# Performance work log

Hardware: AMD Instinct MI355X
Metric: run time of the kernel (lower is better)

Reference implementation:

```python
import jax, jax.numpy as jnp
import numpy as np

N = 4096        # batch size (rows)
K = 4           # instances per class -> num_instances in the torch code
D = 256         # embedding dim
MARGIN = 0.5
SAMPLE_KEY = jax.random.key(42)  # fixed key: deterministic stand-in for torch.multinomial


def setup_inputs() -> dict:
    key = jax.random.key(0)
    x = jax.random.normal(key, (N, D), dtype=jnp.float32)
    # L2-normalize like typical metric-learning embeddings so sims are in [-1, 1]
    inputs = x / jnp.linalg.norm(x, axis=1, keepdims=True)
    targets = (jnp.arange(N) // K).astype(jnp.int32)  # P*K batch: equal-size classes
    return {"inputs": inputs, "targets": targets}


def reference(inputs, targets):
    n = inputs.shape[0]
    km1 = K - 1                 # positives per row
    n_neg = n - K               # negatives per row

    sim = inputs @ inputs.T                                   # [n, n]
    same = targets[:, None] == targets[None, :]
    eye = jnp.eye(n, dtype=bool)
    pos_mask = same & ~eye
    neg_mask = ~same

    # masked_select + per-row sort: masked entries -> +inf, ascending sort,
    # keep first count entries (counts are uniform across rows)
    pos_sorted = jnp.sort(jnp.where(pos_mask, sim, jnp.inf), axis=1)[:, :km1]   # [n, K-1]
    neg_sorted = jnp.sort(jnp.where(neg_mask, sim, jnp.inf), axis=1)[:, :n_neg] # [n, n-K]

    pos_d = jnp.mean(pos_sorted)
    neg_d = jnp.mean(neg_sorted)

    # GaussDistribution per row over negatives
    neg_mean = jnp.mean(neg_sorted, axis=1, keepdims=True)
    neg_std = jnp.sqrt(jnp.mean((neg_sorted - neg_mean) ** 2, axis=1, keepdims=True))
    # NOTE: the original uses exp(+(x-mu)^2 / (2 sigma^2)) (no minus sign) -- faithful
    logprob = (neg_sorted - neg_mean) ** 2 / (2.0 * neg_std ** 2)               # [n, n-K]

    # multinomial without replacement ~ Gumbel top-k on log-weights
    gumbel = -jnp.log(-jnp.log(
        jax.random.uniform(SAMPLE_KEY, logprob.shape, minval=1e-20, maxval=1.0)))
    _, neg_idx = jax.lax.top_k(logprob + gumbel, km1)                            # [n, K-1]
    neg_pair = jnp.take_along_axis(neg_sorted, neg_idx, axis=1)                  # [n, K-1]

    pos_loss = jnp.mean(jnp.log1p(jnp.exp(-2.0 * (pos_sorted - MARGIN))), axis=1)
    neg_loss = 0.04 * jnp.mean(jnp.log1p(jnp.exp(50.0 * (neg_pair - MARGIN))), axis=1)
    loss = jnp.sum(pos_loss + neg_loss) / n

    # prec: fraction of rows where hardest positive > hardest sampled negative + 0.05
    c = jnp.sum(pos_sorted[:, -1] > jnp.max(neg_pair, axis=1) + 0.05)
    prec = c.astype(jnp.float32) / n

    return loss, prec, pos_d, neg_d
```

## Files before the change

kernel.cpp:

```cpp
#include <hip/hip_runtime.h>
#include <hip/hip_bf16.h>
#include <cstdint>
#include <cfloat>
#include <math.h>

#define NN 4096
#define DD 256
#define NNEG 4092
#define MARGIN 0.5f
#define NB 3584
#define NW (NB / 2)

__device__ __forceinline__ uint32_t rotl32(uint32_t x, int r) {
  return (x << r) | (x >> (32 - r));
}

__device__ __forceinline__ void threefry2x32_42(uint32_t x0, uint32_t x1,
                                                uint32_t& o0, uint32_t& o1) {
  const uint32_t k0 = 0u, k1 = 42u;
  const uint32_t k2 = k0 ^ k1 ^ 0x1BD11BDAu;
  x0 += k0; x1 += k1;
#define TF_R(r) { x0 += x1; x1 = rotl32(x1, r); x1 ^= x0; }
  TF_R(13) TF_R(15) TF_R(26) TF_R(6)
  x0 += k1; x1 += k2 + 1u;
  TF_R(17) TF_R(29) TF_R(16) TF_R(24)
  x0 += k2; x1 += k0 + 2u;
  TF_R(13) TF_R(15) TF_R(26) TF_R(6)
  x0 += k0; x1 += k1 + 3u;
  TF_R(17) TF_R(29) TF_R(16) TF_R(24)
  x0 += k1; x1 += k2 + 4u;
  TF_R(13) TF_R(15) TF_R(26) TF_R(6)
  x0 += k2; x1 += k0 + 5u;
#undef TF_R
  o0 = x0; o1 = x1;
}

__device__ __forceinline__ float gumbel_at(uint32_t f) {
  uint32_t o0, o1;
  threefry2x32_42(0u, f, o0, o1);
  uint32_t bits = o0 ^ o1;
  uint32_t fb = (bits >> 9) | 0x3F800000u;
  float fl = __uint_as_float(fb) - 1.0f;
  float u = fmaxf(1e-20f, fl + 1e-20f);
  return -logf(-logf(u));
}

__device__ __forceinline__ int bucket_of(float v) {
  return (int)fminf(fmaxf((v + 0.5f) * (float)NB, 0.0f), (float)(NB - 1));
}

#define BT 128
#define NT (NN / BT)
#define BK 32
#define LDSS 36
#define GEMM_BLOCKS (NT * (NT + 1) / 2)
#define GUMBEL_BLOCKS 240
#define GTOTAL ((uint32_t)NN * (uint32_t)NNEG)

__global__ __launch_bounds__(256) void gemm_gumbel(const float* __restrict__ X,
                                                   float* __restrict__ S,
                                                   float* __restrict__ G) {
  __shared__ float As[BT * LDSS];
  __shared__ float Bs[BT * LDSS];
  const int tid = threadIdx.x;

  if (blockIdx.x >= GEMM_BLOCKS) {
    uint32_t i = (uint32_t)(blockIdx.x - GEMM_BLOCKS) * 256u + (uint32_t)tid;
    const uint32_t stride = (uint32_t)GUMBEL_BLOCKS * 256u;
    for (; i < GTOTAL; i += stride) G[i] = gumbel_at(i);
    return;
  }

  const int tx = tid & 15, ty = tid >> 4;

  int b = blockIdx.x, bi = 0;
  while (b >= NT - bi) { b -= NT - bi; bi++; }
  const int bj = bi + b;
  const int rowBase = bi * BT, colBase = bj * BT;

  float acc[8][8] = {};
  for (int kb = 0; kb < DD; kb += BK) {
#pragma unroll
    for (int it = 0; it < 4; ++it) {
      int idx = tid + 256 * it;
      int r = idx >> 3, c4 = idx & 7;
      float4 av = *(const float4*)(X + (size_t)(rowBase + r) * DD + kb + c4 * 4);
      float4 bv = *(const float4*)(X + (size_t)(colBase + r) * DD + kb + c4 * 4);
      *(float4*)(As + r * LDSS + c4 * 4) = av;
      *(float4*)(Bs + r * LDSS + c4 * 4) = bv;
    }
    __syncthreads();
    for (int k = 0; k < BK; k += 4) {
      float4 a[8], bfr[8];
#pragma unroll
      for (int i = 0; i < 8; ++i) a[i] = *(const float4*)(As + (ty + 16 * i) * LDSS + k);
#pragma unroll
      for (int j = 0; j < 8; ++j) bfr[j] = *(const float4*)(Bs + (tx + 16 * j) * LDSS + k);
#pragma unroll
      for (int i = 0; i < 8; ++i)
#pragma unroll
        for (int j = 0; j < 8; ++j) {
          acc[i][j] += a[i].x * bfr[j].x;
          acc[i][j] += a[i].y * bfr[j].y;
          acc[i][j] += a[i].z * bfr[j].z;
          acc[i][j] += a[i].w * bfr[j].w;
        }
    }
    __syncthreads();
  }
#pragma unroll
  for (int i = 0; i < 8; ++i)
#pragma unroll
    for (int j = 0; j < 8; ++j)
      S[(size_t)(rowBase + ty + 16 * i) * NN + colBase + tx + 16 * j] = acc[i][j];
  if (bi != bj) {
#pragma unroll
    for (int i = 0; i < 8; ++i)
#pragma unroll
      for (int j = 0; j < 8; ++j)
        S[(size_t)(colBase + tx + 16 * j) * NN + rowBase + ty + 16 * i] = acc[i][j];
  }
}

#define INSERT3(sc, v)                                              \
  if ((sc) > s2) {                                                  \
    if ((sc) > s1) {                                                \
      s2 = s1; v2 = v1;                                             \
      if ((sc) > s0) { s1 = s0; v1 = v0; s0 = (sc); v0 = (v); }     \
      else           { s1 = (sc); v1 = (v); }                       \
    } else { s2 = (sc); v2 = (v); }                                 \
  }

template <int USE_G>
__global__ __launch_bounds__(256) void row_kernel(const float* __restrict__ S,
                                                  const float* __restrict__ G,
                                                  float* __restrict__ acc) {
  __shared__ uint32_t histw[NW];
  __shared__ uint32_t offsw[NW];
  __shared__ float sval[NN];
  __shared__ float sh[48];
  __shared__ uint32_t wtot[4];

  const int row = blockIdx.x;
  const int tid = threadIdx.x;
  const int lane = tid & 63, wid = tid >> 6;

#pragma unroll
  for (int i = 0; i < 7; ++i) histw[tid + 256 * i] = 0u;

  const float4* src = (const float4*)(S + (size_t)row * NN);
  const int pslot = row >> 2;
  float vv[16];
#pragma unroll
  for (int it = 0; it < 4; ++it) {
    int slot = tid + 256 * it;
    float4 t4 = src[slot];
    if (slot == pslot) {
      sh[16] = t4.x; sh[17] = t4.y; sh[18] = t4.z; sh[19] = t4.w;
      t4.x = INFINITY; t4.y = INFINITY; t4.z = INFINITY; t4.w = INFINITY;
    }
    vv[4 * it + 0] = t4.x; vv[4 * it + 1] = t4.y;
    vv[4 * it + 2] = t4.z; vv[4 * it + 3] = t4.w;
  }

  float s = 0.0f;
#pragma unroll
  for (int e = 0; e < 16; ++e) if (vv[e] < 1e30f) s += vv[e];
#pragma unroll
  for (int off = 32; off > 0; off >>= 1) s += __shfl_down(s, off, 64);
  if (lane == 0) sh[5 + wid] = s;
  __syncthreads();

#pragma unroll
  for (int e = 0; e < 16; ++e) {
    int b = bucket_of(vv[e]);
    atomicAdd(&histw[b >> 1], 1u << ((b & 1) << 4));
  }
  if (tid == 0) {
    int self = row & 3;
    float p[3]; int m = 0;
#pragma unroll
    for (int c = 0; c < 4; ++c)
      if (c != self) p[m++] = sh[16 + c];
    float t;
    if (p[0] > p[1]) { t = p[0]; p[0] = p[1]; p[1] = t; }
    if (p[1] > p[2]) { t = p[1]; p[1] = p[2]; p[2] = t; }
    if (p[0] > p[1]) { t = p[0]; p[0] = p[1]; p[1] = t; }
    sh[0] = p[0]; sh[1] = p[1]; sh[2] = p[2];
    float tot = sh[5] + sh[6] + sh[7] + sh[8];
    sh[9] = tot;
    sh[3] = tot / (float)NNEG;
  }
  __syncthreads();

  uint32_t hw[7];
  uint32_t s14 = 0;
#pragma unroll
  for (int j = 0; j < 7; ++j) {
    hw[j] = histw[7 * tid + j];
    s14 += (hw[j] & 0xFFFFu) + (hw[j] >> 16);
  }
  uint32_t inc = s14;
#pragma unroll
  for (int off = 1; off < 64; off <<= 1) {
    uint32_t n = __shfl_up(inc, (unsigned)off, 64);
    if (lane >= off) inc += n;
  }
  if (lane == 63) wtot[wid] = inc;

  const float mu = sh[3];
  float q = 0.0f;
#pragma unroll
  for (int e = 0; e < 16; ++e)
    if (vv[e] < 1e30f) { float d = vv[e] - mu; q += d * d; }
#pragma unroll
  for (int off = 32; off > 0; off >>= 1) q += __shfl_down(q, off, 64);
  if (lane == 0) sh[10 + wid] = q;
  __syncthreads();

  uint32_t wbase = 0;
  for (int w = 0; w < wid; ++w) wbase += wtot[w];
  uint32_t run = wbase + inc - s14;
#pragma unroll
  for (int j = 0; j < 7; ++j) {
    uint32_t lo = run; run += hw[j] & 0xFFFFu;
    uint32_t hi = run; run += hw[j] >> 16;
    offsw[7 * tid + j] = lo | (hi << 16);
  }
  if (tid == 0) {
    float var = (sh[10] + sh[11] + sh[12] + sh[13]) / (float)NNEG;
    float sd = sqrtf(var);
    sh[4] = 1.0f / (2.0f * sd * sd);
  }
  __syncthreads();

#pragma unroll
  for (int e = 0; e < 16; ++e) {
    int b = bucket_of(vv[e]);
    uint32_t old = atomicAdd(&offsw[b >> 1], 1u << ((b & 1) << 4));
    uint32_t sl = (old >> ((b & 1) << 4)) & 0xFFFFu;
    sval[sl] = vv[e];
  }
  __syncthreads();

  const float inv2s2 = sh[4];
  const uint32_t fbase = (uint32_t)row * (uint32_t)NNEG;
  const float* __restrict__ Grow = G + fbase;
  float s0 = -FLT_MAX, s1 = -FLT_MAX, s2 = -FLT_MAX;
  float v0 = 0.0f, v1 = 0.0f, v2 = 0.0f;
  float vr[16]; uint32_t cr[16];
#pragma unroll
  for (int it = 0; it < 16; ++it) {
    int sl = tid + 256 * it;
    float v = sval[sl];
    uint32_t cnt = 0u;
    if (v < 1e30f) {
      int b = bucket_of(v);
      uint32_t sh16 = (uint32_t)((b & 1) << 4);
      uint32_t end = (offsw[b >> 1] >> sh16) & 0xFFFFu;
      uint32_t cntb = (histw[b >> 1] >> sh16) & 0xFFFFu;
      uint32_t st = end - cntb;
      int c = (int)st;
      for (uint32_t u = st; u < end; ++u) {
        float w = sval[u];
        c += (w < v || (w == v && (int)u < sl)) ? 1 : 0;
      }
      cnt = (uint32_t)c;
    }
    vr[it] = v; cr[it] = cnt;
  }

#pragma unroll
  for (int it = 0; it < 16; ++it) {
    float v = vr[it];
    if (v < 1e30f) {
      float g = USE_G ? Grow[cr[it]] : gumbel_at(fbase + cr[it]);
      float d = v - mu;
      float sc = d * d * inv2s2 + g;
      INSERT3(sc, v)
    }
  }

#pragma unroll
  for (int dlt = 1; dlt < 64; dlt <<= 1) {
    float t0 = __shfl_xor(s0, dlt, 64), u0 = __shfl_xor(v0, dlt, 64);
    float t1 = __shfl_xor(s1, dlt, 64), u1 = __shfl_xor(v1, dlt, 64);
    float t2 = __shfl_xor(s2, dlt, 64), u2 = __shfl_xor(v2, dlt, 64);
    INSERT3(t0, u0)
    INSERT3(t1, u1)
    INSERT3(t2, u2)
  }
  if (lane == 0) {
    int b0 = 24 + wid * 6;
    sh[b0 + 0] = s0; sh[b0 + 1] = v0;
    sh[b0 + 2] = s1; sh[b0 + 3] = v1;
    sh[b0 + 4] = s2; sh[b0 + 5] = v2;
  }
  __syncthreads();

  if (tid == 0) {
    float g0 = -FLT_MAX, g1 = -FLT_MAX, g2 = -FLT_MAX;
    float w0 = 0.0f, w1 = 0.0f, w2 = 0.0f;
    {
      float s0 = g0, s1 = g1, s2 = g2, v0 = w0, v1 = w1, v2 = w2;
#pragma unroll
      for (int i = 0; i < 12; ++i) {
        float sc = sh[24 + 2 * i], v = sh[24 + 2 * i + 1];
        INSERT3(sc, v)
      }
      g0 = s0; g1 = s1; g2 = s2; w0 = v0; w1 = v1; w2 = v2;
    }
    float negmax = fmaxf(w0, fmaxf(w1, w2));
    float neg_loss = 0.04f * (log1pf(expf(50.0f * (w0 - MARGIN))) +
                              log1pf(expf(50.0f * (w1 - MARGIN))) +
                              log1pf(expf(50.0f * (w2 - MARGIN)))) / 3.0f;
    float p0 = sh[0], p1 = sh[1], p2 = sh[2];
    float pos_loss = (log1pf(expf(-2.0f * (p0 - MARGIN))) +
                      log1pf(expf(-2.0f * (p1 - MARGIN))) +
                      log1pf(expf(-2.0f * (p2 - MARGIN)))) / 3.0f;
    atomicAdd(&acc[0], pos_loss + neg_loss);
    if (p2 > negmax + 0.05f) atomicAdd(&acc[1], 1.0f);
    atomicAdd(&acc[2], p0 + p1 + p2);
    atomicAdd(&acc[3], sh[9]);
  }
}

__global__ void finalize(const float* __restrict__ acc, float* out) {
  if (threadIdx.x == 0 && blockIdx.x == 0) {
    out[0] = acc[0] / 4096.0f;
    out[1] = acc[1] / 4096.0f;
    out[2] = acc[2] / (4096.0f * 3.0f);
    out[3] = acc[3] / (4096.0f * 4092.0f);
  }
}

extern "C" void kernel_launch(void* const* d_in, const int* in_sizes, int n_in,
                              void* d_out, int out_size, void* d_ws, size_t ws_size,
                              hipStream_t stream) {
  (void)in_sizes; (void)n_in; (void)out_size;
  const float* X = (const float*)d_in[0];
  float* S = (float*)d_ws;
  float* acc = (float*)((char*)d_ws + (size_t)NN * NN * 4);
  float* G = (float*)((char*)d_ws + (size_t)NN * NN * 4 + 256);
  const size_t need = (size_t)NN * NN * 4 + 256 + (size_t)GTOTAL * 4;
  const bool have_g = ws_size >= need;

  hipMemsetAsync(acc, 0, 4 * sizeof(float), stream);
  if (have_g) {
    gemm_gumbel<<<GEMM_BLOCKS + GUMBEL_BLOCKS, 256, 0, stream>>>(X, S, G);
    row_kernel<1><<<NN, 256, 0, stream>>>(S, G, acc);
  } else {
    gemm_gumbel<<<GEMM_BLOCKS, 256, 0, stream>>>(X, S, G);
    row_kernel<0><<<NN, 256, 0, stream>>>(S, G, acc);
  }
  finalize<<<1, 64, 0, stream>>>(acc, (float*)d_out);
}
```

Measured before the change: 374.8 us.

## Shrink GEMM tiles, front-load Gumbel blocks, narrow buckets, vectorize rank scan

The symmetric GEMM tile drops from 128 to 64 with a deeper K slice, producing many more, smaller blocks. Gumbel-generation blocks move to the front of the grid and their count rises. The bucket mapping now covers a narrower value range [-0.28, 0.28] at higher resolution, which shrinks per-bucket scan lengths, and the within-bucket rank count reads float4s from LDS and is fused with the Gumbel lookup and top-3 insert. The narrow bucket range assumes the similarity distribution of the test inputs; values outside it are clamped into the edge buckets, which still stays correct but scans more there.

```diff
diff --git a/kernel.cpp b/kernel.cpp
--- a/kernel.cpp
+++ b/kernel.cpp
@@ -10,6 +10,7 @@
 #define MARGIN 0.5f
 #define NB 3584
 #define NW (NB / 2)
+#define GTOTAL ((uint32_t)NN * (uint32_t)NNEG)
 
 __device__ __forceinline__ uint32_t rotl32(uint32_t x, int r) {
   return (x << r) | (x >> (32 - r));
@@ -46,17 +47,17 @@
 }
 
 __device__ __forceinline__ int bucket_of(float v) {
-  return (int)fminf(fmaxf((v + 0.5f) * (float)NB, 0.0f), (float)(NB - 1));
-}
-
-#define BT 128
-#define NT (NN / BT)
-#define BK 32
-#define LDSS 36
-#define GEMM_BLOCKS (NT * (NT + 1) / 2)
-#define GUMBEL_BLOCKS 240
-#define GTOTAL ((uint32_t)NN * (uint32_t)NNEG)
-
+  return (int)fminf(fmaxf((v + 0.28f) * 6400.0f, 0.0f), (float)(NB - 1));
+}
+
+#define BT 64
+#define NTT (NN / BT)
+#define GEMM_BLOCKS (NTT * (NTT + 1) / 2)
+#define BK 64
+#define LDSS 68
+#define GUMBEL_BLOCKS 384
+
+template <int GOFF>
 __global__ __launch_bounds__(256) void gemm_gumbel(const float* __restrict__ X,
                                                    float* __restrict__ S,
                                                    float* __restrict__ G) {
@@ -64,26 +65,26 @@
   __shared__ float Bs[BT * LDSS];
   const int tid = threadIdx.x;
 
-  if (blockIdx.x >= GEMM_BLOCKS) {
-    uint32_t i = (uint32_t)(blockIdx.x - GEMM_BLOCKS) * 256u + (uint32_t)tid;
-    const uint32_t stride = (uint32_t)GUMBEL_BLOCKS * 256u;
+  if (GOFF > 0 && (int)blockIdx.x < GOFF) {
+    uint32_t i = (uint32_t)blockIdx.x * 256u + (uint32_t)tid;
+    const uint32_t stride = (uint32_t)GOFF * 256u;
     for (; i < GTOTAL; i += stride) G[i] = gumbel_at(i);
     return;
   }
 
   const int tx = tid & 15, ty = tid >> 4;
 
-  int b = blockIdx.x, bi = 0;
-  while (b >= NT - bi) { b -= NT - bi; bi++; }
+  int b = (int)blockIdx.x - GOFF, bi = 0;
+  while (b >= NTT - bi) { b -= NTT - bi; bi++; }
   const int bj = bi + b;
   const int rowBase = bi * BT, colBase = bj * BT;
 
-  float acc[8][8] = {};
+  float acc[4][4] = {};
   for (int kb = 0; kb < DD; kb += BK) {
 #pragma unroll
     for (int it = 0; it < 4; ++it) {
       int idx = tid + 256 * it;
-      int r = idx >> 3, c4 = idx & 7;
+      int r = idx >> 4, c4 = idx & 15;
       float4 av = *(const float4*)(X + (size_t)(rowBase + r) * DD + kb + c4 * 4);
       float4 bv = *(const float4*)(X + (size_t)(colBase + r) * DD + kb + c4 * 4);
       *(float4*)(As + r * LDSS + c4 * 4) = av;
@@ -91,15 +92,15 @@
     }
     __syncthreads();
     for (int k = 0; k < BK; k += 4) {
-      float4 a[8], bfr[8];
-#pragma unroll
-      for (int i = 0; i < 8; ++i) a[i] = *(const float4*)(As + (ty + 16 * i) * LDSS + k);
-#pragma unroll
-      for (int j = 0; j < 8; ++j) bfr[j] = *(const float4*)(Bs + (tx + 16 * j) * LDSS + k);
-#pragma unroll
-      for (int i = 0; i < 8; ++i)
-#pragma unroll
-        for (int j = 0; j < 8; ++j) {
+      float4 a[4], bfr[4];
+#pragma unroll
+      for (int i = 0; i < 4; ++i) a[i] = *(const float4*)(As + (ty + 16 * i) * LDSS + k);
+#pragma unroll
+      for (int j = 0; j < 4; ++j) bfr[j] = *(const float4*)(Bs + (tx + 16 * j) * LDSS + k);
+#pragma unroll
+      for (int i = 0; i < 4; ++i)
+#pragma unroll
+        for (int j = 0; j < 4; ++j) {
           acc[i][j] += a[i].x * bfr[j].x;
           acc[i][j] += a[i].y * bfr[j].y;
           acc[i][j] += a[i].z * bfr[j].z;
@@ -109,15 +110,15 @@
     __syncthreads();
   }
 #pragma unroll
-  for (int i = 0; i < 8; ++i)
-#pragma unroll
-    for (int j = 0; j < 8; ++j)
+  for (int i = 0; i < 4; ++i)
+#pragma unroll
+    for (int j = 0; j < 4; ++j)
       S[(size_t)(rowBase + ty + 16 * i) * NN + colBase + tx + 16 * j] = acc[i][j];
   if (bi != bj) {
 #pragma unroll
-    for (int i = 0; i < 8; ++i)
-#pragma unroll
-      for (int j = 0; j < 8; ++j)
+    for (int i = 0; i < 4; ++i)
+#pragma unroll
+      for (int j = 0; j < 4; ++j)
         S[(size_t)(colBase + tx + 16 * j) * NN + rowBase + ty + 16 * i] = acc[i][j];
   }
 }
@@ -137,7 +138,7 @@
                                                   float* __restrict__ acc) {
   __shared__ uint32_t histw[NW];
   __shared__ uint32_t offsw[NW];
-  __shared__ float sval[NN];
+  __shared__ __align__(16) float sval[NN];
   __shared__ float sh[48];
   __shared__ uint32_t wtot[4];
 
@@ -248,36 +249,61 @@
   const float* __restrict__ Grow = G + fbase;
   float s0 = -FLT_MAX, s1 = -FLT_MAX, s2 = -FLT_MAX;
   float v0 = 0.0f, v1 = 0.0f, v2 = 0.0f;
-  float vr[16]; uint32_t cr[16];
+
+  float va[16]; uint32_t sten[16];
+#pragma unroll
+  for (int it = 0; it < 16; ++it) va[it] = sval[tid + 256 * it];
 #pragma unroll
   for (int it = 0; it < 16; ++it) {
-    int sl = tid + 256 * it;
-    float v = sval[sl];
-    uint32_t cnt = 0u;
+    float v = va[it];
+    uint32_t pk = 0u;
     if (v < 1e30f) {
       int b = bucket_of(v);
       uint32_t sh16 = (uint32_t)((b & 1) << 4);
       uint32_t end = (offsw[b >> 1] >> sh16) & 0xFFFFu;
-      uint32_t cntb = (histw[b >> 1] >> sh16) & 0xFFFFu;
-      uint32_t st = end - cntb;
-      int c = (int)st;
-      for (uint32_t u = st; u < end; ++u) {
-        float w = sval[u];
-        c += (w < v || (w == v && (int)u < sl)) ? 1 : 0;
+      uint32_t cb = (histw[b >> 1] >> sh16) & 0xFFFFu;
+      pk = (end - cb) | (end << 16);
+    }
+    sten[it] = pk;
+  }
+
+#pragma unroll
+  for (int half = 0; half < 2; ++half) {
+    float4 w0[8];
+#pragma unroll
+    for (int j = 0; j < 8; ++j) {
+      uint32_t st = sten[half * 8 + j] & 0xFFFFu;
+      w0[j] = *(const float4*)(sval + (st & ~3u));
+    }
+#pragma unroll
+    for (int j = 0; j < 8; ++j) {
+      const int it = half * 8 + j;
+      float v = va[it];
+      if (v < 1e30f) {
+        const int sl = tid + 256 * it;
+        const uint32_t st = sten[it] & 0xFFFFu, en = sten[it] >> 16;
+        const uint32_t nb = en - st;
+        const uint32_t u0 = st & ~3u;
+        int cnt = (int)st;
+        {
+          float4 w = w0[j];
+          cnt += ((u0 + 0 - st) < nb && (w.x < v || (w.x == v && (int)(u0 + 0) < sl))) ? 1 : 0;
+          cnt += ((u0 + 1 - st) < nb && (w.y < v || (w.y == v && (int)(u0 + 1) < sl))) ? 1 : 0;
+          cnt += ((u0 + 2 - st) < nb && (w.z < v || (w.z == v && (int)(u0 + 2) < sl))) ? 1 : 0;
+          cnt += ((u0 + 3 - st) < nb && (w.w < v || (w.w == v && (int)(u0 + 3) < sl))) ? 1 : 0;
+        }
+        for (uint32_t u = u0 + 4; u < en; u += 4) {
+          float4 w = *(const float4*)(sval + u);
+          cnt += ((u + 0 - st) < nb && (w.x < v || (w.x == v && (int)(u + 0) < sl))) ? 1 : 0;
+          cnt += ((u + 1 - st) < nb && (w.y < v || (w.y == v && (int)(u + 1) < sl))) ? 1 : 0;
+          cnt += ((u + 2 - st) < nb && (w.z < v || (w.z == v && (int)(u + 2) < sl))) ? 1 : 0;
+          cnt += ((u + 3 - st) < nb && (w.w < v || (w.w == v && (int)(u + 3) < sl))) ? 1 : 0;
+        }
+        float g = USE_G ? Grow[cnt] : gumbel_at(fbase + (uint32_t)cnt);
+        float d = v - mu;
+        float sc = d * d * inv2s2 + g;
+        INSERT3(sc, v)
       }
-      cnt = (uint32_t)c;
-    }
-    vr[it] = v; cr[it] = cnt;
-  }
-
-#pragma unroll
-  for (int it = 0; it < 16; ++it) {
-    float v = vr[it];
-    if (v < 1e30f) {
-      float g = USE_G ? Grow[cr[it]] : gumbel_at(fbase + cr[it]);
-      float d = v - mu;
-      float sc = d * d * inv2s2 + g;
-      INSERT3(sc, v)
     }
   }
 
@@ -347,10 +373,10 @@
 
   hipMemsetAsync(acc, 0, 4 * sizeof(float), stream);
   if (have_g) {
-    gemm_gumbel<<<GEMM_BLOCKS + GUMBEL_BLOCKS, 256, 0, stream>>>(X, S, G);
+    gemm_gumbel<GUMBEL_BLOCKS><<<GUMBEL_BLOCKS + GEMM_BLOCKS, 256, 0, stream>>>(X, S, G);
     row_kernel<1><<<NN, 256, 0, stream>>>(S, G, acc);
   } else {
-    gemm_gumbel<<<GEMM_BLOCKS, 256, 0, stream>>>(X, S, G);
+    gemm_gumbel<0><<<GEMM_BLOCKS, 256, 0, stream>>>(X, S, G);
     row_kernel<0><<<NN, 256, 0, stream>>>(S, G, acc);
   }
   finalize<<<1, 64, 0, stream>>>(acc, (float*)d_out);
```

Measured after the change: 375.0 us. Within noise of the previous version (+0.1%).

## Rework GEMM tiling, row kernel to 1024 threads, and bucket-owned ranking

Applied to the files above, without the earlier changes.

The GEMM changes from 128x128 symmetric tiles to 64-row by 256-column strips. Each thread owns one column, A rows are read straight from global memory, and the transposed copy is written with float4 stores. The row kernel moves from 256 to 1024 threads per row, uses 4096 histogram buckets over a narrower value range, and makes each thread rank the elements of the buckets it owns instead of the elements it owns. Gumbel blocks are now placed first in the grid. The aim is shorter per-thread serial work and better GEMM write coalescing, at the cost of redundant global A loads, possible load imbalance when values cluster in a few buckets, and a serial 48-entry final merge.

```diff
diff --git a/kernel.cpp b/kernel.cpp
--- a/kernel.cpp
+++ b/kernel.cpp
@@ -8,8 +8,7 @@
 #define DD 256
 #define NNEG 4092
 #define MARGIN 0.5f
-#define NB 3584
-#define NW (NB / 2)
+#define GTOTAL ((uint32_t)NN * (uint32_t)NNEG)
 
 __device__ __forceinline__ uint32_t rotl32(uint32_t x, int r) {
   return (x << r) | (x >> (32 - r));
@@ -45,80 +44,77 @@
   return -logf(-logf(u));
 }
 
+#define NB 4096
+#define NW (NB / 2)
 __device__ __forceinline__ int bucket_of(float v) {
-  return (int)fminf(fmaxf((v + 0.5f) * (float)NB, 0.0f), (float)(NB - 1));
-}
-
-#define BT 128
-#define NT (NN / BT)
-#define BK 32
-#define LDSS 36
-#define GEMM_BLOCKS (NT * (NT + 1) / 2)
-#define GUMBEL_BLOCKS 240
-#define GTOTAL ((uint32_t)NN * (uint32_t)NNEG)
-
+  return (int)fminf(fmaxf((v + 0.28f) * 7314.2857f, 0.0f), (float)(NB - 1));
+}
+
+#define RT 64
+#define CT 256
+#define GBK 32
+#define BKP 36
+#define TRI_BLOCKS 544
+#define GUMBEL_BLOCKS 256
+
+template <int GOFF>
 __global__ __launch_bounds__(256) void gemm_gumbel(const float* __restrict__ X,
                                                    float* __restrict__ S,
                                                    float* __restrict__ G) {
-  __shared__ float As[BT * LDSS];
-  __shared__ float Bs[BT * LDSS];
+  __shared__ float Bs[CT * BKP];
   const int tid = threadIdx.x;
 
-  if (blockIdx.x >= GEMM_BLOCKS) {
-    uint32_t i = (uint32_t)(blockIdx.x - GEMM_BLOCKS) * 256u + (uint32_t)tid;
-    const uint32_t stride = (uint32_t)GUMBEL_BLOCKS * 256u;
+  if (GOFF > 0 && (int)blockIdx.x < GOFF) {
+    uint32_t i = (uint32_t)blockIdx.x * 256u + (uint32_t)tid;
+    const uint32_t stride = (uint32_t)GOFF * 256u;
     for (; i < GTOTAL; i += stride) G[i] = gumbel_at(i);
     return;
   }
 
-  const int tx = tid & 15, ty = tid >> 4;
-
-  int b = blockIdx.x, bi = 0;
-  while (b >= NT - bi) { b -= NT - bi; bi++; }
-  const int bj = bi + b;
-  const int rowBase = bi * BT, colBase = bj * BT;
-
-  float acc[8][8] = {};
-  for (int kb = 0; kb < DD; kb += BK) {
-#pragma unroll
-    for (int it = 0; it < 4; ++it) {
-      int idx = tid + 256 * it;
-      int r = idx >> 3, c4 = idx & 7;
-      float4 av = *(const float4*)(X + (size_t)(rowBase + r) * DD + kb + c4 * 4);
-      float4 bv = *(const float4*)(X + (size_t)(colBase + r) * DD + kb + c4 * 4);
-      *(float4*)(As + r * LDSS + c4 * 4) = av;
-      *(float4*)(Bs + r * LDSS + c4 * 4) = bv;
+  int L = (int)blockIdx.x - GOFF;
+  int bj = 0;
+  while (L >= 2 * (bj + 1) * (bj + 2)) bj++;
+  const int bi = L - 2 * bj * (bj + 1);
+  const int rowBase = bi * RT, colBase = bj * CT;
+
+  const int col = tid;
+  const float* __restrict__ Xc = X + (size_t)(colBase + col) * DD;
+  const float* __restrict__ Xa = X + (size_t)rowBase * DD;
+
+  float acc[RT];
+#pragma unroll
+  for (int r = 0; r < RT; ++r) acc[r] = 0.0f;
+
+  for (int kb = 0; kb < DD; kb += GBK) {
+#pragma unroll
+    for (int q = 0; q < GBK / 4; ++q) {
+      float4 bv = *(const float4*)(Xc + kb + 4 * q);
+      *(float4*)(&Bs[col * BKP + 4 * q]) = bv;
     }
     __syncthreads();
-    for (int k = 0; k < BK; k += 4) {
-      float4 a[8], bfr[8];
-#pragma unroll
-      for (int i = 0; i < 8; ++i) a[i] = *(const float4*)(As + (ty + 16 * i) * LDSS + k);
-#pragma unroll
-      for (int j = 0; j < 8; ++j) bfr[j] = *(const float4*)(Bs + (tx + 16 * j) * LDSS + k);
-#pragma unroll
-      for (int i = 0; i < 8; ++i)
-#pragma unroll
-        for (int j = 0; j < 8; ++j) {
-          acc[i][j] += a[i].x * bfr[j].x;
-          acc[i][j] += a[i].y * bfr[j].y;
-          acc[i][j] += a[i].z * bfr[j].z;
-          acc[i][j] += a[i].w * bfr[j].w;
-        }
+#pragma unroll
+    for (int kk = 0; kk < GBK; kk += 4) {
+      float4 bv = *(const float4*)(&Bs[col * BKP + kk]);
+#pragma unroll
+      for (int r = 0; r < RT; ++r) {
+        float4 av = *(const float4*)(Xa + r * DD + kb + kk);
+        acc[r] += av.x * bv.x;
+        acc[r] += av.y * bv.y;
+        acc[r] += av.z * bv.z;
+        acc[r] += av.w * bv.w;
+      }
     }
     __syncthreads();
   }
-#pragma unroll
-  for (int i = 0; i < 8; ++i)
-#pragma unroll
-    for (int j = 0; j < 8; ++j)
-      S[(size_t)(rowBase + ty + 16 * i) * NN + colBase + tx + 16 * j] = acc[i][j];
-  if (bi != bj) {
-#pragma unroll
-    for (int i = 0; i < 8; ++i)
-#pragma unroll
-      for (int j = 0; j < 8; ++j)
-        S[(size_t)(colBase + tx + 16 * j) * NN + rowBase + ty + 16 * i] = acc[i][j];
+
+#pragma unroll
+  for (int r = 0; r < RT; ++r)
+    S[(size_t)(rowBase + r) * NN + colBase + col] = acc[r];
+#pragma unroll
+  for (int r = 0; r < RT; r += 4) {
+    float4 t;
+    t.x = acc[r]; t.y = acc[r + 1]; t.z = acc[r + 2]; t.w = acc[r + 3];
+    *(float4*)(S + (size_t)(colBase + col) * NN + rowBase + r) = t;
   }
 }
 
@@ -132,47 +128,42 @@
   }
 
 template <int USE_G>
-__global__ __launch_bounds__(256) void row_kernel(const float* __restrict__ S,
-                                                  const float* __restrict__ G,
-                                                  float* __restrict__ acc) {
+__global__ __launch_bounds__(1024) void row_kernel(const float* __restrict__ S,
+                                                   const float* __restrict__ G,
+                                                   float* __restrict__ acc) {
   __shared__ uint32_t histw[NW];
   __shared__ uint32_t offsw[NW];
-  __shared__ float sval[NN];
-  __shared__ float sh[48];
-  __shared__ uint32_t wtot[4];
+  __shared__ __align__(16) float sval[NN];
+  __shared__ float sh[160];
+  __shared__ uint32_t wtot[16];
 
   const int row = blockIdx.x;
   const int tid = threadIdx.x;
   const int lane = tid & 63, wid = tid >> 6;
 
-#pragma unroll
-  for (int i = 0; i < 7; ++i) histw[tid + 256 * i] = 0u;
+  histw[tid] = 0u;
+  histw[tid + 1024] = 0u;
 
   const float4* src = (const float4*)(S + (size_t)row * NN);
   const int pslot = row >> 2;
-  float vv[16];
-#pragma unroll
-  for (int it = 0; it < 4; ++it) {
-    int slot = tid + 256 * it;
-    float4 t4 = src[slot];
-    if (slot == pslot) {
-      sh[16] = t4.x; sh[17] = t4.y; sh[18] = t4.z; sh[19] = t4.w;
-      t4.x = INFINITY; t4.y = INFINITY; t4.z = INFINITY; t4.w = INFINITY;
-    }
-    vv[4 * it + 0] = t4.x; vv[4 * it + 1] = t4.y;
-    vv[4 * it + 2] = t4.z; vv[4 * it + 3] = t4.w;
-  }
+  float4 t4 = src[tid];
+  if (tid == pslot) {
+    sh[16] = t4.x; sh[17] = t4.y; sh[18] = t4.z; sh[19] = t4.w;
+    t4.x = INFINITY; t4.y = INFINITY; t4.z = INFINITY; t4.w = INFINITY;
+  }
+  float vv[4];
+  vv[0] = t4.x; vv[1] = t4.y; vv[2] = t4.z; vv[3] = t4.w;
 
   float s = 0.0f;
 #pragma unroll
-  for (int e = 0; e < 16; ++e) if (vv[e] < 1e30f) s += vv[e];
+  for (int e = 0; e < 4; ++e) if (vv[e] < 1e30f) s += vv[e];
 #pragma unroll
   for (int off = 32; off > 0; off >>= 1) s += __shfl_down(s, off, 64);
-  if (lane == 0) sh[5 + wid] = s;
-  __syncthreads();
-
-#pragma unroll
-  for (int e = 0; e < 16; ++e) {
+  if (lane == 0) sh[32 + wid] = s;
+  __syncthreads();
+
+#pragma unroll
+  for (int e = 0; e < 4; ++e) {
     int b = bucket_of(vv[e]);
     atomicAdd(&histw[b >> 1], 1u << ((b & 1) << 4));
   }
@@ -187,20 +178,17 @@
     if (p[1] > p[2]) { t = p[1]; p[1] = p[2]; p[2] = t; }
     if (p[0] > p[1]) { t = p[0]; p[0] = p[1]; p[1] = t; }
     sh[0] = p[0]; sh[1] = p[1]; sh[2] = p[2];
-    float tot = sh[5] + sh[6] + sh[7] + sh[8];
+    float tot = 0.0f;
+#pragma unroll
+    for (int w = 0; w < 16; ++w) tot += sh[32 + w];
     sh[9] = tot;
     sh[3] = tot / (float)NNEG;
   }
   __syncthreads();
 
-  uint32_t hw[7];
-  uint32_t s14 = 0;
-#pragma unroll
-  for (int j = 0; j < 7; ++j) {
-    hw[j] = histw[7 * tid + j];
-    s14 += (hw[j] & 0xFFFFu) + (hw[j] >> 16);
-  }
-  uint32_t inc = s14;
+  uint32_t hw0 = histw[2 * tid], hw1 = histw[2 * tid + 1];
+  uint32_t s4 = (hw0 & 0xFFFFu) + (hw0 >> 16) + (hw1 & 0xFFFFu) + (hw1 >> 16);
+  uint32_t inc = s4;
 #pragma unroll
   for (int off = 1; off < 64; off <<= 1) {
     uint32_t n = __shfl_up(inc, (unsigned)off, 64);
@@ -211,31 +199,36 @@
   const float mu = sh[3];
   float q = 0.0f;
 #pragma unroll
-  for (int e = 0; e < 16; ++e)
+  for (int e = 0; e < 4; ++e)
     if (vv[e] < 1e30f) { float d = vv[e] - mu; q += d * d; }
 #pragma unroll
   for (int off = 32; off > 0; off >>= 1) q += __shfl_down(q, off, 64);
-  if (lane == 0) sh[10 + wid] = q;
+  if (lane == 0) sh[48 + wid] = q;
   __syncthreads();
 
   uint32_t wbase = 0;
   for (int w = 0; w < wid; ++w) wbase += wtot[w];
-  uint32_t run = wbase + inc - s14;
-#pragma unroll
-  for (int j = 0; j < 7; ++j) {
-    uint32_t lo = run; run += hw[j] & 0xFFFFu;
-    uint32_t hi = run; run += hw[j] >> 16;
-    offsw[7 * tid + j] = lo | (hi << 16);
+  uint32_t run = wbase + inc - s4;
+  {
+    uint32_t lo0 = run; run += hw0 & 0xFFFFu;
+    uint32_t hi0 = run; run += hw0 >> 16;
+    offsw[2 * tid] = lo0 | (hi0 << 16);
+    uint32_t lo1 = run; run += hw1 & 0xFFFFu;
+    uint32_t hi1 = run; run += hw1 >> 16;
+    offsw[2 * tid + 1] = lo1 | (hi1 << 16);
   }
   if (tid == 0) {
-    float var = (sh[10] + sh[11] + sh[12] + sh[13]) / (float)NNEG;
+    float var = 0.0f;
+#pragma unroll
+    for (int w = 0; w < 16; ++w) var += sh[48 + w];
+    var /= (float)NNEG;
     float sd = sqrtf(var);
     sh[4] = 1.0f / (2.0f * sd * sd);
   }
   __syncthreads();
 
 #pragma unroll
-  for (int e = 0; e < 16; ++e) {
+  for (int e = 0; e < 4; ++e) {
     int b = bucket_of(vv[e]);
     uint32_t old = atomicAdd(&offsw[b >> 1], 1u << ((b & 1) << 4));
     uint32_t sl = (old >> ((b & 1) << 4)) & 0xFFFFu;
@@ -245,39 +238,28 @@
 
   const float inv2s2 = sh[4];
   const uint32_t fbase = (uint32_t)row * (uint32_t)NNEG;
-  const float* __restrict__ Grow = G + fbase;
   float s0 = -FLT_MAX, s1 = -FLT_MAX, s2 = -FLT_MAX;
   float v0 = 0.0f, v1 = 0.0f, v2 = 0.0f;
-  float vr[16]; uint32_t cr[16];
-#pragma unroll
-  for (int it = 0; it < 16; ++it) {
-    int sl = tid + 256 * it;
-    float v = sval[sl];
-    uint32_t cnt = 0u;
-    if (v < 1e30f) {
-      int b = bucket_of(v);
-      uint32_t sh16 = (uint32_t)((b & 1) << 4);
-      uint32_t end = (offsw[b >> 1] >> sh16) & 0xFFFFu;
-      uint32_t cntb = (histw[b >> 1] >> sh16) & 0xFFFFu;
-      uint32_t st = end - cntb;
-      int c = (int)st;
-      for (uint32_t u = st; u < end; ++u) {
-        float w = sval[u];
-        c += (w < v || (w == v && (int)u < sl)) ? 1 : 0;
+#pragma unroll
+  for (int m = 0; m < 4; ++m) {
+    const int b = tid + 1024 * m;
+    const uint32_t shft = (uint32_t)((b & 1) << 4);
+    const uint32_t en = (offsw[b >> 1] >> shft) & 0xFFFFu;
+    const uint32_t cb = (histw[b >> 1] >> shft) & 0xFFFFu;
+    const uint32_t st = en - cb;
+    for (uint32_t u = st; u < en; ++u) {
+      float v = sval[u];
+      if (v < 1e30f) {
+        uint32_t rk = st;
+        for (uint32_t u2 = st; u2 < en; ++u2) {
+          float w = sval[u2];
+          rk += (w < v || (w == v && u2 < u)) ? 1u : 0u;
+        }
+        float g = USE_G ? G[fbase + rk] : gumbel_at(fbase + rk);
+        float d = v - mu;
+        float sc = d * d * inv2s2 + g;
+        INSERT3(sc, v)
       }
-      cnt = (uint32_t)c;
-    }
-    vr[it] = v; cr[it] = cnt;
-  }
-
-#pragma unroll
-  for (int it = 0; it < 16; ++it) {
-    float v = vr[it];
-    if (v < 1e30f) {
-      float g = USE_G ? Grow[cr[it]] : gumbel_at(fbase + cr[it]);
-      float d = v - mu;
-      float sc = d * d * inv2s2 + g;
-      INSERT3(sc, v)
     }
   }
 
@@ -291,7 +273,7 @@
     INSERT3(t2, u2)
   }
   if (lane == 0) {
-    int b0 = 24 + wid * 6;
+    int b0 = 64 + wid * 6;
     sh[b0 + 0] = s0; sh[b0 + 1] = v0;
     sh[b0 + 2] = s1; sh[b0 + 3] = v1;
     sh[b0 + 4] = s2; sh[b0 + 5] = v2;
@@ -303,9 +285,8 @@
     float w0 = 0.0f, w1 = 0.0f, w2 = 0.0f;
     {
       float s0 = g0, s1 = g1, s2 = g2, v0 = w0, v1 = w1, v2 = w2;
-#pragma unroll
-      for (int i = 0; i < 12; ++i) {
-        float sc = sh[24 + 2 * i], v = sh[24 + 2 * i + 1];
+      for (int i = 0; i < 48; ++i) {
+        float sc = sh[64 + 2 * i], v = sh[64 + 2 * i + 1];
         INSERT3(sc, v)
       }
       g0 = s0; g1 = s1; g2 = s2; w0 = v0; w1 = v1; w2 = v2;
@@ -347,11 +328,11 @@
 
   hipMemsetAsync(acc, 0, 4 * sizeof(float), stream);
   if (have_g) {
-    gemm_gumbel<<<GEMM_BLOCKS + GUMBEL_BLOCKS, 256, 0, stream>>>(X, S, G);
-    row_kernel<1><<<NN, 256, 0, stream>>>(S, G, acc);
+    gemm_gumbel<GUMBEL_BLOCKS><<<GUMBEL_BLOCKS + TRI_BLOCKS, 256, 0, stream>>>(X, S, G);
+    row_kernel<1><<<NN, 1024, 0, stream>>>(S, G, acc);
   } else {
-    gemm_gumbel<<<GEMM_BLOCKS, 256, 0, stream>>>(X, S, G);
-    row_kernel<0><<<NN, 256, 0, stream>>>(S, G, acc);
+    gemm_gumbel<0><<<TRI_BLOCKS, 256, 0, stream>>>(X, S, G);
+    row_kernel<0><<<NN, 1024, 0, stream>>>(S, G, acc);
   }
   finalize<<<1, 64, 0, stream>>>(acc, (float*)d_out);
 }
```

Result: slower. 1.126 ms (+200.5%).
